# Kernel optimization log

Measured on AMD Instinct MI355X. Metric: run time of the kernel, lower is better.

The kernel has to match this reference:

```python
import jax, jax.numpy as jnp
import numpy as np

B, S, HID = 2, 2048, 2048
NH, NKV, HD = 16, 8, 256
EPS = 1e-6
SCALE = 256 ** -0.5  # query_pre_attn_scalar ** -0.5


def setup_inputs() -> dict:
    key = jax.random.key(0)
    k1, k2, k3 = jax.random.split(key, 3)
    hidden_states = jax.random.normal(k1, (B, S, HID), dtype=jnp.float32)
    w_qkv = jax.random.normal(k2, (HID, (NH + 2 * NKV) * HD), dtype=jnp.float32) * 0.02
    w_o = jax.random.normal(k3, (NH * HD, HID), dtype=jnp.float32) * 0.02
    q_norm_w = jnp.zeros((HD,), dtype=jnp.float32)  # Gemma RMSNorm uses (1 + w)
    k_norm_w = jnp.zeros((HD,), dtype=jnp.float32)
    # Real rotary tables: inv_freq over half dim, emb = concat(freqs, freqs)
    inv_freq = 1.0 / (10000.0 ** (jnp.arange(0, HD, 2, dtype=jnp.float32) / HD))
    pos = jnp.arange(S, dtype=jnp.float32)
    freqs = pos[:, None] * inv_freq[None, :]            # [S, HD/2]
    emb = jnp.concatenate([freqs, freqs], axis=-1)       # [S, HD]
    cos = jnp.broadcast_to(jnp.cos(emb)[None], (B, S, HD))
    sin = jnp.broadcast_to(jnp.sin(emb)[None], (B, S, HD))
    return {"hidden_states": hidden_states, "cos": cos, "sin": sin,
            "w_qkv": w_qkv, "w_o": w_o, "q_norm_w": q_norm_w, "k_norm_w": k_norm_w}


def _rms_norm(x, w):
    # Gemma3RMSNorm: fp32 rms, scale by (1 + w)
    xf = x.astype(jnp.float32)
    var = jnp.mean(xf * xf, axis=-1, keepdims=True)
    out = xf * jax.lax.rsqrt(var + EPS) * (1.0 + w.astype(jnp.float32))
    return out.astype(x.dtype)


def _rotate_half(x):
    x1, x2 = jnp.split(x, 2, axis=-1)
    return jnp.concatenate([-x2, x1], axis=-1)


def reference(hidden_states, cos, sin, w_qkv, w_o, q_norm_w, k_norm_w):
    qkv = jnp.einsum("bsh,hf->bsf", hidden_states, w_qkv)
    q, k, v = jnp.split(qkv, [NH * HD, NH * HD + NKV * HD], axis=-1)
    q = q.reshape(B, S, NH, HD).transpose(0, 2, 1, 3)    # [b, nh, s, d]
    k = k.reshape(B, S, NKV, HD).transpose(0, 2, 1, 3)   # [b, nkv, s, d]
    v = v.reshape(B, S, NKV, HD).transpose(0, 2, 1, 3)
    q = _rms_norm(q, q_norm_w)
    k = _rms_norm(k, k_norm_w)
    c = cos[:, None, :, :]  # broadcast over heads
    s = sin[:, None, :, :]
    q = q * c + _rotate_half(q) * s
    k = k * c + _rotate_half(k) * s
    n_rep = NH // NKV
    k = jnp.repeat(k, n_rep, axis=1)  # GQA expand: [b, nh, s, d]
    v = jnp.repeat(v, n_rep, axis=1)
    scores = jnp.einsum("bhqd,bhkd->bhqk", q, k) * SCALE
    attn = jax.nn.softmax(scores, axis=-1)
    out = jnp.einsum("bhqk,bhkd->bhqd", attn, v)
    out = out.transpose(0, 2, 1, 3).reshape(B, S, NH * HD)
    return jnp.einsum("bsf,fh->bsh", out, w_o)
```

## Files before the change

### kernel.cpp

```cpp
#include <hip/hip_runtime.h>
#include <stdint.h>

typedef __attribute__((ext_vector_type(8))) short short8;
typedef __attribute__((ext_vector_type(4))) short short4v;
typedef __attribute__((ext_vector_type(4))) float f32x4;

#define GLOAD16(gp, lp) __builtin_amdgcn_global_load_lds( \
    (__attribute__((address_space(1))) void*)(gp),        \
    (__attribute__((address_space(3))) void*)(lp), 16, 0, 0)

#define BAR   __builtin_amdgcn_s_barrier()
#define LGKM0 asm volatile("s_waitcnt lgkmcnt(0)" ::: "memory")
#define VMCNT4 asm volatile("s_waitcnt vmcnt(4)" ::: "memory")

__device__ __forceinline__ unsigned short f2bf(float f) {
    union { float f; unsigned u; } v; v.f = f;
    unsigned u = v.u + 0x7fffu + ((v.u >> 16) & 1u);
    return (unsigned short)(u >> 16);
}
__device__ __forceinline__ float bf2f(short s) {
    union { unsigned u; float f; } v;
    v.u = ((unsigned)(unsigned short)s) << 16;
    return v.f;
}

__global__ __launch_bounds__(256) void cvt_f32_bf16(const float* __restrict__ in,
                                                    short* __restrict__ out) {
    const int i = (blockIdx.x * 256 + threadIdx.x) * 4;
    const float4 v = *(const float4*)(in + i);
    short4v o;
    o[0] = (short)f2bf(v.x); o[1] = (short)f2bf(v.y);
    o[2] = (short)f2bf(v.z); o[3] = (short)f2bf(v.w);
    *(short4v*)(out + i) = o;
}

__global__ __launch_bounds__(256) void transpose_cvt(const float* __restrict__ in,
                                                     short* __restrict__ out,
                                                     int R, int C) {
    __shared__ float tile[64 * 65];
    const int t = threadIdx.x;
    const int r0 = blockIdx.y * 64, c0 = blockIdx.x * 64;
    const int rl = t >> 4, cl4 = (t & 15) * 4;
#pragma unroll
    for (int rep = 0; rep < 4; rep++) {
        const int r = rep * 16 + rl;
        const float4 v = *(const float4*)(in + (long)(r0 + r) * C + c0 + cl4);
        tile[r * 65 + cl4 + 0] = v.x;
        tile[r * 65 + cl4 + 1] = v.y;
        tile[r * 65 + cl4 + 2] = v.z;
        tile[r * 65 + cl4 + 3] = v.w;
    }
    __syncthreads();
#pragma unroll
    for (int rep = 0; rep < 4; rep++) {
        const int cc = rep * 16 + rl;
        short4v o;
#pragma unroll
        for (int j = 0; j < 4; j++) o[j] = (short)f2bf(tile[(cl4 + j) * 65 + cc]);
        *(short4v*)(out + (long)(c0 + cc) * R + r0 + cl4) = o;
    }
}

__global__ __launch_bounds__(256) void vtrans(const short* __restrict__ QKV,
                                              short* __restrict__ Vt) {
    __shared__ short tile[64 * 72];
    const int t = threadIdx.x;
    const int s0 = blockIdx.x * 64, d0 = blockIdx.y * 64;
    const int hb = blockIdx.z >> 1, b = blockIdx.z & 1;
    const short* src = QKV + ((long)(24 + hb) * 4096 + b * 2048) * 256;
    short* dst = Vt + (long)blockIdx.z * 256 * 2048;
#pragma unroll
    for (int p = 0; p < 2; p++) {
        const int c = p * 256 + t;
        const int r = c >> 3, col8 = (c & 7) * 8;
        *(short8*)(tile + r * 72 + col8) = *(const short8*)(src + (long)(s0 + r) * 256 + d0 + col8);
    }
    __syncthreads();
#pragma unroll
    for (int p = 0; p < 2; p++) {
        const int c = p * 256 + t;
        const int dr = c >> 3, sc8 = (c & 7) * 8;
        short8 o;
#pragma unroll
        for (int j = 0; j < 8; j++) o[j] = tile[(sc8 + j) * 72 + dr];
        *(short8*)(dst + (long)(d0 + dr) * 2048 + s0 + sc8) = o;
    }
}

template<int N, int K, int OUTMODE>
__global__ __launch_bounds__(256) void gemm_nt(const short* __restrict__ A,
                                               const short* __restrict__ Bt,
                                               void* __restrict__ Cv) {
    __shared__ __align__(16) short Al[128 * 32];
    __shared__ __align__(16) short Bl[128 * 32];
    const int t = threadIdx.x;
    const int lane = t & 63, w = t >> 6;
    const int quad = lane >> 4, l16 = lane & 15;
    const int wr = w >> 1, wc = w & 1;
    const long m0 = (long)blockIdx.y * 128, n0 = (long)blockIdx.x * 128;

    const short* Ag0 = A + (m0 + (t >> 2)) * K + (t & 3) * 8;
    const short* Bg0 = Bt + (n0 + (t >> 2)) * K + (t & 3) * 8;

    f32x4 acc[4][4] = {};

    for (int k0 = 0; k0 < K; k0 += 32) {
        __syncthreads();
        GLOAD16(Ag0 + k0,            Al + t * 8);
        GLOAD16(Ag0 + 64 * K + k0,   Al + (t + 256) * 8);
        GLOAD16(Bg0 + k0,            Bl + t * 8);
        GLOAD16(Bg0 + 64 * K + k0,   Bl + (t + 256) * 8);
        __syncthreads();
        short8 af[4], bfr[4];
#pragma unroll
        for (int i = 0; i < 4; i++)
            af[i] = *(const short8*)(Al + (wr * 64 + i * 16 + l16) * 32 + quad * 8);
#pragma unroll
        for (int i = 0; i < 4; i++)
            bfr[i] = *(const short8*)(Bl + (wc * 64 + i * 16 + l16) * 32 + quad * 8);
#pragma unroll
        for (int mi = 0; mi < 4; mi++)
#pragma unroll
            for (int ni = 0; ni < 4; ni++)
                acc[mi][ni] = __builtin_amdgcn_mfma_f32_16x16x32_bf16(af[mi], bfr[ni], acc[mi][ni], 0, 0, 0);
    }

    const long crow = m0 + wr * 64 + quad * 4;
    const long ccol = n0 + wc * 64 + l16;
    if constexpr (OUTMODE == 0) {
        float* C = (float*)Cv;
#pragma unroll
        for (int mi = 0; mi < 4; mi++)
#pragma unroll
            for (int ni = 0; ni < 4; ni++)
#pragma unroll
                for (int r = 0; r < 4; r++)
                    C[(crow + mi * 16 + r) * N + ccol + ni * 16] = acc[mi][ni][r];
    } else {
        short* C = (short*)Cv;
#pragma unroll
        for (int mi = 0; mi < 4; mi++)
#pragma unroll
            for (int ni = 0; ni < 4; ni++)
#pragma unroll
                for (int r = 0; r < 4; r++) {
                    const long m = crow + mi * 16 + r;
                    const long f = ccol + ni * 16;
                    C[(f >> 8) * 1048576 + m * 256 + (f & 255)] = (short)f2bf(acc[mi][ni][r]);
                }
    }
}

__global__ __launch_bounds__(512, 2) void gemm256_qkv(const short* __restrict__ A,
                                                      const short* __restrict__ Bt,
                                                      short* __restrict__ QKV) {
    constexpr int K = 2048;
    constexpr int NTM = 31;
    __shared__ __align__(16) short L[2][4][8192];

    const int t = threadIdx.x;
    const int lane = t & 63, w = t >> 6;
    const int quad = lane >> 4, l16 = lane & 15;
    const int wr = w >> 2, wc = w & 3;
    const int bh = 2 + (wc >> 1);
    const int brow0 = (wc & 1) * 64;

    const int flat = blockIdx.y * 32 + blockIdx.x;
    const int swz = (flat & 7) * 64 + (flat >> 3);
    const int bx = swz & 31, by = swz >> 5;
    const long m0 = (long)by * 256, n0 = (long)bx * 256;

    const int r0 = t >> 3, r1 = (512 + t) >> 3;
    const int k0s = ((t & 7) * 8) ^ (((r0 >> 2) & 1) << 4);
    const int k1s = ((t & 7) * 8) ^ (((r1 >> 2) & 1) << 4);
    const short* aS0 = A + (m0 + r0) * K + k0s;
    const short* aS1 = A + (m0 + r1) * K + k1s;
    const short* aT0 = aS0 + 128 * K;
    const short* aT1 = aS1 + 128 * K;
    const short* bS0 = Bt + (n0 + r0) * K + k0s;
    const short* bS1 = Bt + (n0 + r1) * K + k1s;
    const short* bT0 = bS0 + 128 * K;
    const short* bT1 = bS1 + 128 * K;

#define STG(p0, p1, bsel, slot, kt) do {                     \
    const int _ko = ((kt) & NTM) * 64;                       \
    GLOAD16((p0) + _ko, &L[bsel][slot][t * 8]);              \
    GLOAD16((p1) + _ko, &L[bsel][slot][4096 + t * 8]);       \
} while (0)

#define LDA4(bsel, rb) do {                                                        \
    _Pragma("unroll") for (int m = 0; m < 4; ++m) {                                \
        const int _r = (rb) + m * 16 + l16;                                        \
        const int _sw = ((_r >> 2) & 1) << 4;                                      \
        a[m][0] = *(const short8*)(&L[bsel][wr][_r * 64 + ((quad * 8) ^ _sw)]);    \
        a[m][1] = *(const short8*)(&L[bsel][wr][_r * 64 + ((32 + quad * 8) ^ _sw)]); \
    } } while (0)

#define LDB2(bsel, nb) do {                                                        \
    _Pragma("unroll") for (int n = 0; n < 2; ++n) {                                \
        const int _r = brow0 + ((nb) + n) * 16 + l16;                              \
        const int _sw = ((_r >> 2) & 1) << 4;                                      \
        b[(nb) + n][0] = *(const short8*)(&L[bsel][bh][_r * 64 + ((quad * 8) ^ _sw)]); \
        b[(nb) + n][1] = *(const short8*)(&L[bsel][bh][_r * 64 + ((32 + quad * 8) ^ _sw)]); \
    } } while (0)

#define PH_MFMA(MB, NB)                                                            \
    __builtin_amdgcn_s_setprio(1);                                                 \
    _Pragma("unroll") for (int m = 0; m < 4; ++m)                                  \
    _Pragma("unroll") for (int n = 0; n < 2; ++n)                                  \
    _Pragma("unroll") for (int kk = 0; kk < 2; ++kk)                               \
        acc[(MB) + m][(NB) + n] = __builtin_amdgcn_mfma_f32_16x16x32_bf16(         \
            a[m][kk], b[(NB) + n][kk], acc[(MB) + m][(NB) + n], 0, 0, 0);          \
    __builtin_amdgcn_s_setprio(0);

    short8 a[4][2], b[4][2];
    f32x4 acc[8][4] = {};

    STG(aS0, aS1, 0, 0, 0);
    STG(aT0, aT1, 0, 1, 0);
    STG(bS0, bS1, 0, 2, 0);
    STG(bT0, bT1, 0, 3, 0);
    STG(bS0, bS1, 1, 2, 1);
    STG(bT0, bT1, 1, 3, 1);
    VMCNT4;
    BAR;

    for (int it = 0; it < 16; ++it) {
        const int kt0 = 2 * it;
        LDA4(0, 0);
        LDB2(0, 0);
        STG(aS0, aS1, 1, 0, kt0 + 1);
        BAR; LGKM0;
        PH_MFMA(0, 0);
        BAR;
        LDB2(0, 2);
        STG(aT0, aT1, 1, 1, kt0 + 1);
        BAR; LGKM0;
        PH_MFMA(0, 2);
        BAR;
        LDA4(0, 64);
        STG(bS0, bS1, 0, 2, kt0 + 2);
        BAR; LGKM0;
        PH_MFMA(4, 2);
        BAR;
        STG(bT0, bT1, 0, 3, kt0 + 2);
        BAR;
        PH_MFMA(4, 0);
        VMCNT4;
        BAR;
        LDA4(1, 0);
        LDB2(1, 0);
        STG(aS0, aS1, 0, 0, kt0 + 2);
        BAR; LGKM0;
        PH_MFMA(0, 0);
        BAR;
        LDB2(1, 2);
        STG(aT0, aT1, 0, 1, kt0 + 2);
        BAR; LGKM0;
        PH_MFMA(0, 2);
        BAR;
        LDA4(1, 64);
        STG(bS0, bS1, 1, 2, kt0 + 3);
        BAR; LGKM0;
        PH_MFMA(4, 2);
        BAR;
        STG(bT0, bT1, 1, 3, kt0 + 3);
        BAR;
        PH_MFMA(4, 0);
        VMCNT4;
        BAR;
    }

    short* Cp = QKV + (long)bx * 1048576;
    const int cbase = wc * 64;
#pragma unroll
    for (int mi = 0; mi < 8; ++mi)
#pragma unroll
        for (int ni = 0; ni < 4; ++ni)
#pragma unroll
            for (int r = 0; r < 4; ++r) {
                const long m = m0 + wr * 128 + mi * 16 + quad * 4 + r;
                Cp[m * 256 + cbase + ni * 16 + l16] = (short)f2bf(acc[mi][ni][r]);
            }

#undef STG
#undef LDA4
#undef LDB2
#undef PH_MFMA
}

__global__ __launch_bounds__(256) void prep_qk(short* __restrict__ QKV,
                                               const float* __restrict__ cosp,
                                               const float* __restrict__ sinp,
                                               const float* __restrict__ qw,
                                               const float* __restrict__ kw) {
    const int t = threadIdx.x, w = t >> 6, lane = t & 63;
    const int d4 = lane * 4;
    const float sgn = (lane < 32) ? -1.0f : 1.0f;
#pragma unroll
    for (int i = 0; i < 4; i++) {
        const int g = blockIdx.x * 16 + w * 4 + i;
        const int u = g >> 12, m = g & 4095;
        short* rowp = QKV + (long)g * 256;
        const short4v raw = *(const short4v*)(rowp + d4);
        float x[4];
#pragma unroll
        for (int j = 0; j < 4; j++) x[j] = bf2f(raw[j]);
        float ss = x[0]*x[0] + x[1]*x[1] + x[2]*x[2] + x[3]*x[3];
#pragma unroll
        for (int msk = 1; msk < 64; msk <<= 1) ss += __shfl_xor(ss, msk, 64);
        const float rinv = rsqrtf(ss * (1.0f / 256.0f) + 1e-6f);
        const float4 wv = *(const float4*)(((u < 16) ? qw : kw) + d4);
        const float wa[4] = {wv.x, wv.y, wv.z, wv.w};
        const float4 cv = *(const float4*)(cosp + (long)m * 256 + d4);
        const float4 sv = *(const float4*)(sinp + (long)m * 256 + d4);
        const float ca[4] = {cv.x, cv.y, cv.z, cv.w};
        const float sa[4] = {sv.x, sv.y, sv.z, sv.w};
        float n[4];
#pragma unroll
        for (int j = 0; j < 4; j++) n[j] = x[j] * rinv * (1.0f + wa[j]);
        const float scale = (u < 16) ? 0.0625f : 1.0f;
        short4v ov;
#pragma unroll
        for (int j = 0; j < 4; j++) {
            const float p = __shfl_xor(n[j], 32, 64);
            ov[j] = (short)f2bf((n[j] * ca[j] + sgn * p * sa[j]) * scale);
        }
        *(short4v*)(rowp + d4) = ov;
    }
}

__global__ __launch_bounds__(512, 2) void attn(const short* __restrict__ QKV,
                                               const short* __restrict__ Vt,
                                               short* __restrict__ O) {
    __shared__ __align__(16) short Kl[2][64 * 256];
    __shared__ __align__(16) short Vl[256 * 64];
    __shared__ __align__(16) short Pl[128 * 64];
    __shared__ __align__(16) float Ll[128];

    const int t = threadIdx.x, w = t >> 6, lane = t & 63;
    const int quad = lane >> 4, l16 = lane & 15;
    const int q0 = blockIdx.x * 128, h = blockIdx.y, b = blockIdx.z;
    const int kh = h >> 1;
    const short* Qp = QKV + ((long)h * 4096 + b * 2048 + q0) * 256;
    const short* Kp = QKV + ((long)(16 + kh) * 4096 + b * 2048) * 256;
    const short* Vp = Vt + (long)(kh * 2 + b) * 256 * 2048;

    const int qh2 = w >> 1, kh2 = w & 1;
    short8 qf2[2][8];
#pragma unroll
    for (int mi = 0; mi < 2; mi++)
#pragma unroll
        for (int ks = 0; ks < 8; ks++)
            qf2[mi][ks] = *(const short8*)(Qp + (qh2 * 32 + mi * 16 + l16) * 256 + ks * 32 + quad * 8);

    f32x4 acc[4][4] = {};
    float li_[2][4] = {};

    const int qh = w >> 2, dstr = (w & 3) * 64;

#pragma unroll
    for (int i = 0; i < 4; i++) {
        const int c = i * 512 + t;
        const int rK = c >> 5, j = c & 31;
        GLOAD16(Kp + (long)rK * 256 + (j ^ (rK & 31)) * 8, Kl[0] + c * 8);
    }

    for (int kt = 0; kt < 32; kt++) {
        const int k0 = kt * 64;
        __syncthreads();

#pragma unroll
        for (int i = 0; i < 4; i++) {
            const int c = i * 512 + t;
            const int dV = c >> 3, j = c & 7;
            GLOAD16(Vp + (long)dV * 2048 + k0 + (j ^ (dV & 7)) * 8, Vl + c * 8);
        }
        const int kn = ((kt + 1) & 31) * 64;
#pragma unroll
        for (int i = 0; i < 4; i++) {
            const int c = i * 512 + t;
            const int rK = c >> 5, j = c & 31;
            GLOAD16(Kp + (long)(kn + rK) * 256 + (j ^ (rK & 31)) * 8, Kl[(kt + 1) & 1] + c * 8);
        }

        const short* Kb = Kl[kt & 1];
        f32x4 sc[2][2] = {};
        __builtin_amdgcn_s_setprio(1);
#pragma unroll
        for (int ct2 = 0; ct2 < 2; ct2++) {
            const int rowK = kh2 * 32 + ct2 * 16 + l16;
#pragma unroll
            for (int ks = 0; ks < 8; ks++) {
                const int dc = (ks * 4 + quad) ^ (rowK & 31);
                const short8 kf = *(const short8*)(Kb + rowK * 256 + dc * 8);
                sc[0][ct2] = __builtin_amdgcn_mfma_f32_16x16x32_bf16(qf2[0][ks], kf, sc[0][ct2], 0, 0, 0);
                sc[1][ct2] = __builtin_amdgcn_mfma_f32_16x16x32_bf16(qf2[1][ks], kf, sc[1][ct2], 0, 0, 0);
            }
        }
        __builtin_amdgcn_s_setprio(0);

#pragma unroll
        for (int mi = 0; mi < 2; mi++)
#pragma unroll
            for (int ct2 = 0; ct2 < 2; ct2++)
#pragma unroll
                for (int r = 0; r < 4; r++) {
                    const float p = __expf(sc[mi][ct2][r]);
                    li_[mi][r] += p;
                    const int prow = qh2 * 32 + mi * 16 + quad * 4 + r;
                    const int pcol = kh2 * 32 + ct2 * 16 + l16;
                    Pl[prow * 64 + (pcol ^ ((prow & 7) << 3))] = (short)f2bf(p);
                }
        __syncthreads();

        __builtin_amdgcn_s_setprio(1);
#pragma unroll
        for (int k2 = 0; k2 < 2; k2++) {
            short8 pf[4];
#pragma unroll
            for (int mi2 = 0; mi2 < 4; mi2++) {
                const int prow = qh * 64 + mi2 * 16 + l16;
                pf[mi2] = *(const short8*)(Pl + prow * 64 + ((k2 * 32 + quad * 8) ^ ((prow & 7) << 3)));
            }
#pragma unroll
            for (int ni = 0; ni < 4; ni++) {
                const int dV = dstr + ni * 16 + l16;
                const int dc = (k2 * 4 + quad) ^ (dV & 7);
                const short8 vf = *(const short8*)(Vl + dV * 64 + dc * 8);
#pragma unroll
                for (int mi2 = 0; mi2 < 4; mi2++)
                    acc[mi2][ni] = __builtin_amdgcn_mfma_f32_16x16x32_bf16(pf[mi2], vf, acc[mi2][ni], 0, 0, 0);
            }
        }
        __builtin_amdgcn_s_setprio(0);
    }

    float lv_[2][4];
#pragma unroll
    for (int mi = 0; mi < 2; mi++)
#pragma unroll
        for (int r = 0; r < 4; r++) {
            float v = li_[mi][r];
            v += __shfl_xor(v, 1, 64);
            v += __shfl_xor(v, 2, 64);
            v += __shfl_xor(v, 4, 64);
            v += __shfl_xor(v, 8, 64);
            lv_[mi][r] = v;
        }
    __syncthreads();
    if (kh2 == 0 && l16 == 0) {
#pragma unroll
        for (int mi = 0; mi < 2; mi++)
#pragma unroll
            for (int r = 0; r < 4; r++)
                Ll[qh2 * 32 + mi * 16 + quad * 4 + r] = lv_[mi][r];
    }
    __syncthreads();
    if (kh2 == 1 && l16 == 0) {
#pragma unroll
        for (int mi = 0; mi < 2; mi++)
#pragma unroll
            for (int r = 0; r < 4; r++)
                Ll[qh2 * 32 + mi * 16 + quad * 4 + r] += lv_[mi][r];
    }
    __syncthreads();

    short* Op = O + (long)(b * 2048 + q0 + qh * 64) * 4096 + h * 256 + dstr;
#pragma unroll
    for (int mi2 = 0; mi2 < 4; mi2++) {
        const float4 lv = *(const float4*)(Ll + qh * 64 + mi2 * 16 + quad * 4);
        const float inv[4] = {1.0f / lv.x, 1.0f / lv.y, 1.0f / lv.z, 1.0f / lv.w};
#pragma unroll
        for (int ni = 0; ni < 4; ni++)
#pragma unroll
            for (int r = 0; r < 4; r++)
                Op[(long)(mi2 * 16 + quad * 4 + r) * 4096 + ni * 16 + l16] =
                    (short)f2bf(acc[mi2][ni][r] * inv[r]);
    }
}

extern "C" void kernel_launch(void* const* d_in, const int* in_sizes, int n_in,
                              void* d_out, int out_size, void* d_ws, size_t ws_size,
                              hipStream_t stream) {
    const float* hs   = (const float*)d_in[0];
    const float* cosp = (const float*)d_in[1];
    const float* sinp = (const float*)d_in[2];
    const float* wqkv = (const float*)d_in[3];
    const float* wo   = (const float*)d_in[4];
    const float* qnw  = (const float*)d_in[5];
    const float* knw  = (const float*)d_in[6];
    float* out = (float*)d_out;

    short* poolA  = (short*)d_ws;
    short* Xb     = poolA;
    short* Wqkv_t = poolA + (size_t)4096 * 2048;
    short* QKV    = poolA + (size_t)4096 * 2048 + (size_t)8192 * 2048;
    short* Vt     = poolA;
    short* Ob     = poolA + (size_t)16 * 256 * 2048;
    short* Wo_t   = QKV;

    cvt_f32_bf16<<<8192, 256, 0, stream>>>(hs, Xb);
    transpose_cvt<<<dim3(128, 32), 256, 0, stream>>>(wqkv, Wqkv_t, 2048, 8192);
    gemm256_qkv<<<dim3(32, 16), 512, 0, stream>>>(Xb, Wqkv_t, QKV);
    prep_qk<<<6144, 256, 0, stream>>>(QKV, cosp, sinp, qnw, knw);
    vtrans<<<dim3(32, 4, 16), 256, 0, stream>>>(QKV, Vt);
    attn<<<dim3(16, 16, 2), 512, 0, stream>>>(QKV, Vt, Ob);
    transpose_cvt<<<dim3(32, 64), 256, 0, stream>>>(wo, Wo_t, 4096, 2048);
    gemm_nt<2048, 4096, 0><<<dim3(16, 32), 256, 0, stream>>>(Ob, Wo_t, (void*)out);
}
```

Baseline: 585.5 us.

## Remap QK warp tiling to match PV layout and replace syncthreads with explicit waitcnt barriers

Changes the QK^T warp partition so each warp computes 64 query rows by 16 key columns, the same query group it later uses in the PV step. This raises Q fragments held in registers from 16 to 32 short8 values. The two __syncthreads per key tile become raw s_barrier calls with explicit vmcnt/lgkmcnt waits, so the prefetch of the next K tile can stay in flight across the barrier. Row-sum reduction now sums four warps' partials with LDS atomics. The risks are higher register pressure at two blocks per CU, and ordering of the async global-to-LDS loads that depends on hand-counted vmcnt values.

After: 687.8 us. 17.5% more time.

```diff
diff --git a/kernel.cpp b/kernel.cpp
--- a/kernel.cpp
+++ b/kernel.cpp
@@ -10,8 +10,10 @@
     (__attribute__((address_space(3))) void*)(lp), 16, 0, 0)
 
 #define BAR   __builtin_amdgcn_s_barrier()
+#define BARM  asm volatile("s_barrier" ::: "memory")
 #define LGKM0 asm volatile("s_waitcnt lgkmcnt(0)" ::: "memory")
 #define VMCNT4 asm volatile("s_waitcnt vmcnt(4)" ::: "memory")
+#define VMCNT8 asm volatile("s_waitcnt vmcnt(8)" ::: "memory")
 
 __device__ __forceinline__ unsigned short f2bf(float f) {
     union { float f; unsigned u; } v; v.f = f;
@@ -346,18 +348,18 @@
     const short* Kp = QKV + ((long)(16 + kh) * 4096 + b * 2048) * 256;
     const short* Vp = Vt + (long)(kh * 2 + b) * 256 * 2048;
 
-    const int qh2 = w >> 1, kh2 = w & 1;
-    short8 qf2[2][8];
-#pragma unroll
-    for (int mi = 0; mi < 2; mi++)
+    const int qg = w >> 2, kg = w & 3;
+    const int dstr = kg * 64;
+
+    short8 qf4[4][8];
+#pragma unroll
+    for (int mi = 0; mi < 4; mi++)
 #pragma unroll
         for (int ks = 0; ks < 8; ks++)
-            qf2[mi][ks] = *(const short8*)(Qp + (qh2 * 32 + mi * 16 + l16) * 256 + ks * 32 + quad * 8);
+            qf4[mi][ks] = *(const short8*)(Qp + (qg * 64 + mi * 16 + l16) * 256 + ks * 32 + quad * 8);
 
     f32x4 acc[4][4] = {};
-    float li_[2][4] = {};
-
-    const int qh = w >> 2, dstr = (w & 3) * 64;
+    float li_[4][4] = {};
 
 #pragma unroll
     for (int i = 0; i < 4; i++) {
@@ -368,7 +370,7 @@
 
     for (int kt = 0; kt < 32; kt++) {
         const int k0 = kt * 64;
-        __syncthreads();
+        BARM;
 
 #pragma unroll
         for (int i = 0; i < 4; i++) {
@@ -383,36 +385,36 @@
             const int rK = c >> 5, j = c & 31;
             GLOAD16(Kp + (long)(kn + rK) * 256 + (j ^ (rK & 31)) * 8, Kl[(kt + 1) & 1] + c * 8);
         }
+        VMCNT8;
 
         const short* Kb = Kl[kt & 1];
-        f32x4 sc[2][2] = {};
+        const int rowK = kg * 16 + l16;
+        f32x4 sc[4] = {};
         __builtin_amdgcn_s_setprio(1);
 #pragma unroll
-        for (int ct2 = 0; ct2 < 2; ct2++) {
-            const int rowK = kh2 * 32 + ct2 * 16 + l16;
-#pragma unroll
-            for (int ks = 0; ks < 8; ks++) {
-                const int dc = (ks * 4 + quad) ^ (rowK & 31);
-                const short8 kf = *(const short8*)(Kb + rowK * 256 + dc * 8);
-                sc[0][ct2] = __builtin_amdgcn_mfma_f32_16x16x32_bf16(qf2[0][ks], kf, sc[0][ct2], 0, 0, 0);
-                sc[1][ct2] = __builtin_amdgcn_mfma_f32_16x16x32_bf16(qf2[1][ks], kf, sc[1][ct2], 0, 0, 0);
-            }
+        for (int ks = 0; ks < 8; ks++) {
+            const int dc = (ks * 4 + quad) ^ (rowK & 31);
+            const short8 kf = *(const short8*)(Kb + rowK * 256 + dc * 8);
+            sc[0] = __builtin_amdgcn_mfma_f32_16x16x32_bf16(qf4[0][ks], kf, sc[0], 0, 0, 0);
+            sc[1] = __builtin_amdgcn_mfma_f32_16x16x32_bf16(qf4[1][ks], kf, sc[1], 0, 0, 0);
+            sc[2] = __builtin_amdgcn_mfma_f32_16x16x32_bf16(qf4[2][ks], kf, sc[2], 0, 0, 0);
+            sc[3] = __builtin_amdgcn_mfma_f32_16x16x32_bf16(qf4[3][ks], kf, sc[3], 0, 0, 0);
         }
         __builtin_amdgcn_s_setprio(0);
 
 #pragma unroll
-        for (int mi = 0; mi < 2; mi++)
-#pragma unroll
-            for (int ct2 = 0; ct2 < 2; ct2++)
-#pragma unroll
-                for (int r = 0; r < 4; r++) {
-                    const float p = __expf(sc[mi][ct2][r]);
-                    li_[mi][r] += p;
-                    const int prow = qh2 * 32 + mi * 16 + quad * 4 + r;
-                    const int pcol = kh2 * 32 + ct2 * 16 + l16;
-                    Pl[prow * 64 + (pcol ^ ((prow & 7) << 3))] = (short)f2bf(p);
-                }
-        __syncthreads();
+        for (int mi = 0; mi < 4; mi++)
+#pragma unroll
+            for (int r = 0; r < 4; r++) {
+                const float p = __expf(sc[mi][r]);
+                li_[mi][r] += p;
+                const int prow = qg * 64 + mi * 16 + quad * 4 + r;
+                const int pcol = kg * 16 + l16;
+                Pl[prow * 64 + (pcol ^ ((prow & 7) << 3))] = (short)f2bf(p);
+            }
+        LGKM0;
+        VMCNT4;
+        BARM;
 
         __builtin_amdgcn_s_setprio(1);
 #pragma unroll
@@ -420,7 +422,7 @@
             short8 pf[4];
 #pragma unroll
             for (int mi2 = 0; mi2 < 4; mi2++) {
-                const int prow = qh * 64 + mi2 * 16 + l16;
+                const int prow = qg * 64 + mi2 * 16 + l16;
                 pf[mi2] = *(const short8*)(Pl + prow * 64 + ((k2 * 32 + quad * 8) ^ ((prow & 7) << 3)));
             }
 #pragma unroll
@@ -436,9 +438,9 @@
         __builtin_amdgcn_s_setprio(0);
     }
 
-    float lv_[2][4];
-#pragma unroll
-    for (int mi = 0; mi < 2; mi++)
+    float lv_[4][4];
+#pragma unroll
+    for (int mi = 0; mi < 4; mi++)
 #pragma unroll
         for (int r = 0; r < 4; r++) {
             float v = li_[mi][r];
@@ -449,27 +451,27 @@
             lv_[mi][r] = v;
         }
     __syncthreads();
-    if (kh2 == 0 && l16 == 0) {
-#pragma unroll
-        for (int mi = 0; mi < 2; mi++)
+    if (kg == 0 && l16 == 0) {
+#pragma unroll
+        for (int mi = 0; mi < 4; mi++)
 #pragma unroll
             for (int r = 0; r < 4; r++)
-                Ll[qh2 * 32 + mi * 16 + quad * 4 + r] = lv_[mi][r];
+                Ll[qg * 64 + mi * 16 + quad * 4 + r] = lv_[mi][r];
     }
     __syncthreads();
-    if (kh2 == 1 && l16 == 0) {
-#pragma unroll
-        for (int mi = 0; mi < 2; mi++)
+    if (kg != 0 && l16 == 0) {
+#pragma unroll
+        for (int mi = 0; mi < 4; mi++)
 #pragma unroll
             for (int r = 0; r < 4; r++)
-                Ll[qh2 * 32 + mi * 16 + quad * 4 + r] += lv_[mi][r];
+                atomicAdd(&Ll[qg * 64 + mi * 16 + quad * 4 + r], lv_[mi][r]);
     }
     __syncthreads();
 
-    short* Op = O + (long)(b * 2048 + q0 + qh * 64) * 4096 + h * 256 + dstr;
+    short* Op = O + (long)(b * 2048 + q0 + qg * 64) * 4096 + h * 256 + dstr;
 #pragma unroll
     for (int mi2 = 0; mi2 < 4; mi2++) {
-        const float4 lv = *(const float4*)(Ll + qh * 64 + mi2 * 16 + quad * 4);
+        const float4 lv = *(const float4*)(Ll + qg * 64 + mi2 * 16 + quad * 4);
         const float inv[4] = {1.0f / lv.x, 1.0f / lv.y, 1.0f / lv.z, 1.0f / lv.w};
 #pragma unroll
         for (int ni = 0; ni < 4; ni++)
```
